# Performance work log

Hardware: AMD Instinct MI355X
Metric: run time of the kernel (lower is better)

The kernel has to match this reference:

```python
import jax, jax.numpy as jnp
import numpy as np

B, N, M, C, H, W = 8, 16, 4, 2, 256, 256
GAMMA = 0.5   # gamma0
BETA = 1.0    # beta
EPS = 1e-8


def setup_inputs() -> dict:
    key = jax.random.key(0)
    k1, k2, k3, k4 = jax.random.split(key, 4)
    gt_arr = jax.random.randint(k1, (B, M, H, W), 0, C)
    sample_arr = jax.random.uniform(k2, (B, N, C, H, W), dtype=jnp.float32)
    prob = jax.random.uniform(k3, (B, N), dtype=jnp.float32)
    prob_gt = jax.random.uniform(k4, (B, M), dtype=jnp.float32)
    prob_gt = prob_gt / prob_gt.sum(-1, keepdims=True)  # gt mixture weights sum to 1
    sample_shape = jnp.array([4, 4], dtype=jnp.int64 if jax.config.read('jax_enable_x64') else jnp.int32)  # (K,S); unused since G0=1
    return {"gt_arr": gt_arr, "sample_arr": sample_arr, "prob": prob,
            "prob_gt": prob_gt, "sample_shape": sample_shape}


def _cost_iou(sample, gt_oh):
    # sample: (B,N,C,HW), gt_oh: (B,M,C,HW) -> cost (B,N,M)
    inter = jnp.einsum('bnch,bmch->bnmc', sample, gt_oh)
    union = sample.sum(-1)[:, :, None, :] + gt_oh.sum(-1)[:, None, :, :] - inter
    # drop background channel 0, mean over remaining channels
    return 1.0 - ((inter + 1.0) / (union + 1.0))[..., 1:].mean(-1)


def _coupling(cost, prob_gt):
    # Greedy sequential OT coupling (gamma != 1 branch), vectorized per gt column
    # via water-filling over cost-sorted samples; sequential over gt columns.
    Bn, Nn, Mn = cost.shape
    mass = 1.0 / Mn

    def per_batch(cb):  # cb: (N,M)
        order_gt = jnp.argsort(cb.min(axis=0))  # gts by their min cost

        def step(carry, i):
            rowsums, P = carry
            col = cb[:, i]                      # (N,)
            ordj = jnp.argsort(col)             # samples by cost for this gt
            caps = GAMMA - rowsums[ordj]        # remaining capacity, >= 0
            excl = jnp.cumsum(caps) - caps      # exclusive prefix of capacities
            a_sorted = jnp.clip(mass - excl, 0.0, caps)
            assign = jnp.zeros((Nn,), cb.dtype).at[ordj].set(a_sorted)
            P = P.at[:, i].set(assign)
            return (rowsums + assign, P), None

        init = (jnp.zeros((Nn,), cb.dtype), jnp.zeros((Nn, Mn), cb.dtype))
        (_, P), _ = jax.lax.scan(step, init, order_gt)
        return P

    P = jax.vmap(per_batch)(cost)
    return P * (prob_gt * Mn)[:, None, :]


def _forward(gt_arr, sample_arr, prob, prob_gt):
    Bn, Nn, Cn, Hn, Wn = sample_arr.shape
    Mn = gt_arr.shape[1]
    sample = sample_arr.reshape(Bn, Nn, Cn, Hn * Wn)
    gt_oh = jnp.transpose(
        jax.nn.one_hot(gt_arr.reshape(Bn, Mn, Hn * Wn), Cn, dtype=sample.dtype),
        (0, 1, 3, 2))                            # (B,M,C,HW)
    cost = _cost_iou(sample, gt_oh)              # (B,N,M)
    P = jax.lax.stop_gradient(_coupling(jax.lax.stop_gradient(cost), prob_gt))
    seg_loss = (P * cost).sum((1, 2)).mean()
    # KL: F.kl_div(log(prob+eps), target_prob) with 'mean' reduction (xlogy at 0)
    target = P.sum(-1)                           # (B,N)
    logp = jnp.log(prob + EPS)
    safe_t = jnp.where(target > 0, target, 1.0)
    kl = jnp.where(target > 0, target * (jnp.log(safe_t) - logp), 0.0).mean()
    loss = seg_loss + BETA * kl
    return loss, seg_loss, kl


def reference(gt_arr, sample_arr, prob, prob_gt, sample_shape):
    return _forward(gt_arr, sample_arr, prob, prob_gt)
```

## Files before the change

kernel.cpp:

```cpp
#include <hip/hip_runtime.h>
#include <math.h>

static constexpr int Bn = 8;
static constexpr int Nn = 16;
static constexpr int Mn = 4;
static constexpr int Cn = 2;
static constexpr int HWn = 256 * 256;
static constexpr int SEGS = 64;
static constexpr int SEGLEN = HWn / SEGS;
#define GAMMA_F 0.5f
#define MASS_F 0.25f
#define EPS_F 1e-8f


__global__ __launch_bounds__(256) void inter2_kernel(
    const float* __restrict__ sample, const int* __restrict__ gt,
    float* __restrict__ inter_part, float* __restrict__ ssum_part,
    float* __restrict__ gsum_part) {
  int seg = blockIdx.x & (SEGS - 1);
  int b = blockIdx.x >> 6;
  int tid = threadIdx.x;
  int w = tid >> 6;
  int lane = tid & 63;
  size_t segoff = (size_t)seg * SEGLEN;

  const int* gtb = gt + ((size_t)b * Mn) * HWn + segoff;
  const float* sb = sample + (size_t)b * Nn * Cn * HWn + HWn + segoff;

  float ss[4] = {0.f, 0.f, 0.f, 0.f};
  float im[4][4] = {};
  float cnt[4] = {0.f, 0.f, 0.f, 0.f};

#pragma unroll
  for (int q = 0; q < 4; ++q) {
    int idx = q * 64 + lane;
    int4 g0 = reinterpret_cast<const int4*>(gtb + 0 * HWn)[idx];
    int4 g1 = reinterpret_cast<const int4*>(gtb + 1 * HWn)[idx];
    int4 g2 = reinterpret_cast<const int4*>(gtb + 2 * HWn)[idx];
    int4 g3 = reinterpret_cast<const int4*>(gtb + 3 * HWn)[idx];
    float mf[4][4];
    {
      int a0[4] = {g0.x, g0.y, g0.z, g0.w};
      int a1[4] = {g1.x, g1.y, g1.z, g1.w};
      int a2[4] = {g2.x, g2.y, g2.z, g2.w};
      int a3[4] = {g3.x, g3.y, g3.z, g3.w};
#pragma unroll
      for (int e = 0; e < 4; ++e) {
        mf[e][0] = (a0[e] == 1) ? 1.f : 0.f;
        mf[e][1] = (a1[e] == 1) ? 1.f : 0.f;
        mf[e][2] = (a2[e] == 1) ? 1.f : 0.f;
        mf[e][3] = (a3[e] == 1) ? 1.f : 0.f;
      }
    }
#pragma unroll
    for (int m = 0; m < 4; ++m)
      cnt[m] += (mf[0][m] + mf[1][m]) + (mf[2][m] + mf[3][m]);
#pragma unroll
    for (int nn = 0; nn < 4; ++nn) {
      const float* spn = sb + (size_t)(w * 4 + nn) * (Cn * HWn);
      float4 x = reinterpret_cast<const float4*>(spn)[idx];
      float xs[4] = {x.x, x.y, x.z, x.w};
#pragma unroll
      for (int e = 0; e < 4; ++e) {
        float v = xs[e];
        ss[nn] += v;
#pragma unroll
        for (int m = 0; m < 4; ++m) im[nn][m] = fmaf(v, mf[e][m], im[nn][m]);
      }
    }
  }

  __shared__ __align__(16) float red[4][20][68];
  __shared__ __align__(16) float redc[4][68];
#pragma unroll
  for (int nn = 0; nn < 4; ++nn) {
    red[w][nn * 5 + 0][lane] = ss[nn];
#pragma unroll
    for (int m = 0; m < 4; ++m) red[w][nn * 5 + 1 + m][lane] = im[nn][m];
  }
  if (w == 0) {
#pragma unroll
    for (int m = 0; m < 4; ++m) redc[m][lane] = cnt[m];
  }
  __syncthreads();

  if (tid < 80) {
    int rw = tid / 20, v = tid % 20;
    const float4* row = reinterpret_cast<const float4*>(&red[rw][v][0]);
    float4 a4 = row[0];
#pragma unroll
    for (int j = 1; j < 16; ++j) {
      float4 t = row[j];
      a4.x += t.x; a4.y += t.y; a4.z += t.z; a4.w += t.w;
    }
    float s = (a4.x + a4.y) + (a4.z + a4.w);
    int n = rw * 4 + v / 5;
    int k = v % 5;
    int bn = b * Nn + n;
    if (k == 0)
      ssum_part[(size_t)bn * SEGS + seg] = s;
    else
      inter_part[((size_t)bn * Mn + (k - 1)) * SEGS + seg] = s;
  } else if (tid < 84) {
    int m = tid - 80;
    const float4* row = reinterpret_cast<const float4*>(&redc[m][0]);
    float4 a4 = row[0];
#pragma unroll
    for (int j = 1; j < 16; ++j) {
      float4 t = row[j];
      a4.x += t.x; a4.y += t.y; a4.z += t.z; a4.w += t.w;
    }
    float s = (a4.x + a4.y) + (a4.z + a4.w);
    gsum_part[((size_t)b * Mn + m) * SEGS + seg] = s;
  }
}

__global__ __launch_bounds__(256) void finish_kernel(
    const float* __restrict__ inter_part, const float* __restrict__ ssum_part,
    const float* __restrict__ gsum_part,
    const float* __restrict__ prob, const float* __restrict__ prob_gt,
    float* __restrict__ out) {
  __shared__ float s_cost[Bn * Nn * Mn];
  __shared__ float s_ssum[Bn * Nn];
  __shared__ float s_gsum[Bn * Mn];
  __shared__ float s_red[8];
  int tid = threadIdx.x;

  if (tid < Bn * Nn) {
    const float4* row = reinterpret_cast<const float4*>(&ssum_part[(size_t)tid * SEGS]);
    float4 a4 = row[0];
#pragma unroll
    for (int j = 1; j < 16; ++j) {
      float4 t = row[j];
      a4.x += t.x; a4.y += t.y; a4.z += t.z; a4.w += t.w;
    }
    s_ssum[tid] = (a4.x + a4.y) + (a4.z + a4.w);
  } else if (tid < 128 + Bn * Mn) {
    int idx = tid - 128;
    const float4* row = reinterpret_cast<const float4*>(&gsum_part[(size_t)idx * SEGS]);
    float4 a4 = row[0];
#pragma unroll
    for (int j = 1; j < 16; ++j) {
      float4 t = row[j];
      a4.x += t.x; a4.y += t.y; a4.z += t.z; a4.w += t.w;
    }
    s_gsum[idx] = (a4.x + a4.y) + (a4.z + a4.w);
  }
  __syncthreads();

  for (int idx = tid; idx < Bn * Nn * Mn; idx += 256) {
    int m = idx & 3;
    int bn = idx >> 2;
    int b = bn >> 4;
    const float4* row = reinterpret_cast<const float4*>(&inter_part[(size_t)idx * SEGS]);
    float4 a4 = row[0];
#pragma unroll
    for (int j = 1; j < 16; ++j) {
      float4 t = row[j];
      a4.x += t.x; a4.y += t.y; a4.z += t.z; a4.w += t.w;
    }
    float inter = (a4.x + a4.y) + (a4.z + a4.w);
    float uni = s_ssum[bn] + s_gsum[(b << 2) + m] - inter;
    s_cost[idx] = 1.0f - (inter + 1.0f) / (uni + 1.0f);
  }
  __syncthreads();

  float seg_part = 0.f, kl_part = 0.f;
  if (tid < Bn * Nn) {
    int b = tid >> 4;
    int n = tid & 15;
    int base = (tid & 63) & ~15;

    float4 cv = *reinterpret_cast<const float4*>(&s_cost[tid * Mn]);
    float cc0 = cv.x, cc1 = cv.y, cc2 = cv.z, cc3 = cv.w;
    float pg0 = prob_gt[b * Mn + 0], pg1 = prob_gt[b * Mn + 1];
    float pg2 = prob_gt[b * Mn + 2], pg3 = prob_gt[b * Mn + 3];

    float m0 = cc0, m1 = cc1, m2 = cc2, m3 = cc3;
#pragma unroll
    for (int off = 1; off < 16; off <<= 1) {
      m0 = fminf(m0, __shfl_xor(m0, off));
      m1 = fminf(m1, __shfl_xor(m1, off));
      m2 = fminf(m2, __shfl_xor(m2, off));
      m3 = fminf(m3, __shfl_xor(m3, off));
    }
    int r0 = (m1 < m0) + (m2 < m0) + (m3 < m0);
    int r1 = (m0 <= m1) + (m2 < m1) + (m3 < m1);
    int r2 = (m0 <= m2) + (m1 <= m2) + (m3 < m2);
    int r3 = (m0 <= m3) + (m1 <= m3) + (m2 <= m3);

    float rowsum = 0.f;
    float target = 0.f;
#pragma unroll
    for (int k = 0; k < Mn; ++k) {
      int i = (r0 == k) ? 0 : (r1 == k) ? 1 : (r2 == k) ? 2 : 3;
      float v = (i == 0) ? cc0 : (i == 1) ? cc1 : (i == 2) ? cc2 : cc3;
      float pg = (i == 0) ? pg0 : (i == 1) ? pg1 : (i == 2) ? pg2 : pg3;
      float cap = GAMMA_F - rowsum;
      float excl = 0.f;
#pragma unroll 4
      for (int j = 0; j < Nn; ++j) {
        float vj = __shfl(v, base + j);
        float capj = __shfl(cap, base + j);
        bool pred = (vj < v) || (vj == v && j < n);
        excl += pred ? capj : 0.f;
      }
      float a = fminf(fmaxf(MASS_F - excl, 0.f), cap);
      rowsum += a;
      float p = a * pg * (float)Mn;
      seg_part += p * v;
      target += p;
    }
    kl_part = (target > 0.f)
                  ? target * (logf(target) - logf(prob[tid] + EPS_F))
                  : 0.f;
  }

#pragma unroll
  for (int off = 32; off > 0; off >>= 1) {
    seg_part += __shfl_down(seg_part, off);
    kl_part += __shfl_down(kl_part, off);
  }
  int lane = tid & 63, wv = tid >> 6;
  if (lane == 0) { s_red[wv * 2] = seg_part; s_red[wv * 2 + 1] = kl_part; }
  __syncthreads();
  if (tid == 0) {
    float seg = 0.f, kl = 0.f;
    for (int w = 0; w < 4; ++w) { seg += s_red[w * 2]; kl += s_red[w * 2 + 1]; }
    seg /= (float)Bn;
    kl /= (float)(Bn * Nn);
    out[0] = seg + 1.0f * kl;
    out[1] = seg;
    out[2] = kl;
  }
}

extern "C" void kernel_launch(void* const* d_in, const int* in_sizes, int n_in,
                              void* d_out, int out_size, void* d_ws, size_t ws_size,
                              hipStream_t stream) {
  const int* gt = (const int*)d_in[0];
  const float* sample = (const float*)d_in[1];
  const float* prob = (const float*)d_in[2];
  const float* prob_gt = (const float*)d_in[3];
  float* out = (float*)d_out;

  char* ws = (char*)d_ws;
  float* inter_part = (float*)(ws + 0);
  float* ssum_part = (float*)(ws + 131072);
  float* gsum_part = (float*)(ws + 163840);

  inter2_kernel<<<Bn * SEGS, 256, 0, stream>>>(sample, gt, inter_part, ssum_part, gsum_part);
  finish_kernel<<<1, 256, 0, stream>>>(inter_part, ssum_part, gsum_part, prob, prob_gt, out);
}
```

Measured before the change: 23.29 us.

## Fuse partial-reduction and finish kernels via cooperative grid sync

Merges the two kernels into one cooperative launch: all blocks write partial sums into a single packed workspace, synchronize with a grid barrier, then block 0 performs the final reduction and greedy coupling. The final row reduction is restructured to use float4 loads with shuffle reductions across 16 lanes. This is meant to remove the second kernel launch and its launch gap, at the cost of a grid-wide barrier and a cooperative launch that requires all 512 blocks to be co-resident.

```diff
diff --git a/kernel.cpp b/kernel.cpp
--- a/kernel.cpp
+++ b/kernel.cpp
@@ -1,5 +1,8 @@
 #include <hip/hip_runtime.h>
+#include <hip/hip_cooperative_groups.h>
 #include <math.h>
+
+namespace cg = cooperative_groups;
 
 static constexpr int Bn = 8;
 static constexpr int Nn = 16;
@@ -12,11 +15,12 @@
 #define MASS_F 0.25f
 #define EPS_F 1e-8f
 
-
-__global__ __launch_bounds__(256) void inter2_kernel(
+static constexpr int ROWS = 672;
+
+__global__ __launch_bounds__(256) void fused_kernel(
     const float* __restrict__ sample, const int* __restrict__ gt,
-    float* __restrict__ inter_part, float* __restrict__ ssum_part,
-    float* __restrict__ gsum_part) {
+    const float* __restrict__ prob, const float* __restrict__ prob_gt,
+    float* __restrict__ part, float* __restrict__ out) {
   int seg = blockIdx.x & (SEGS - 1);
   int b = blockIdx.x >> 6;
   int tid = threadIdx.x;
@@ -97,10 +101,8 @@
     int n = rw * 4 + v / 5;
     int k = v % 5;
     int bn = b * Nn + n;
-    if (k == 0)
-      ssum_part[(size_t)bn * SEGS + seg] = s;
-    else
-      inter_part[((size_t)bn * Mn + (k - 1)) * SEGS + seg] = s;
+    int r = (k == 0) ? (512 + bn) : (bn * Mn + (k - 1));
+    part[(size_t)r * SEGS + seg] = s;
   } else if (tid < 84) {
     int m = tid - 80;
     const float4* row = reinterpret_cast<const float4*>(&redc[m][0]);
@@ -111,70 +113,51 @@
       a4.x += t.x; a4.y += t.y; a4.z += t.z; a4.w += t.w;
     }
     float s = (a4.x + a4.y) + (a4.z + a4.w);
-    gsum_part[((size_t)b * Mn + m) * SEGS + seg] = s;
-  }
-}
-
-__global__ __launch_bounds__(256) void finish_kernel(
-    const float* __restrict__ inter_part, const float* __restrict__ ssum_part,
-    const float* __restrict__ gsum_part,
-    const float* __restrict__ prob, const float* __restrict__ prob_gt,
-    float* __restrict__ out) {
+    part[(size_t)(640 + b * Mn + m) * SEGS + seg] = s;
+  }
+
+  cg::this_grid().sync();
+
+  if (blockIdx.x != 0) return;
+
+  __shared__ float rows[ROWS];
   __shared__ float s_cost[Bn * Nn * Mn];
-  __shared__ float s_ssum[Bn * Nn];
-  __shared__ float s_gsum[Bn * Mn];
   __shared__ float s_red[8];
-  int tid = threadIdx.x;
-
-  if (tid < Bn * Nn) {
-    const float4* row = reinterpret_cast<const float4*>(&ssum_part[(size_t)tid * SEGS]);
-    float4 a4 = row[0];
-#pragma unroll
-    for (int j = 1; j < 16; ++j) {
-      float4 t = row[j];
-      a4.x += t.x; a4.y += t.y; a4.z += t.z; a4.w += t.w;
-    }
-    s_ssum[tid] = (a4.x + a4.y) + (a4.z + a4.w);
-  } else if (tid < 128 + Bn * Mn) {
-    int idx = tid - 128;
-    const float4* row = reinterpret_cast<const float4*>(&gsum_part[(size_t)idx * SEGS]);
-    float4 a4 = row[0];
-#pragma unroll
-    for (int j = 1; j < 16; ++j) {
-      float4 t = row[j];
-      a4.x += t.x; a4.y += t.y; a4.z += t.z; a4.w += t.w;
-    }
-    s_gsum[idx] = (a4.x + a4.y) + (a4.z + a4.w);
+  int wv = tid >> 6;
+
+#pragma unroll 2
+  for (int it = 0; it < ROWS / 16; ++it) {
+    int r0 = it * 16 + wv * 4;
+    float4 x = reinterpret_cast<const float4*>(part)[(size_t)r0 * 16 + lane];
+    float s = (x.x + x.y) + (x.z + x.w);
+    s += __shfl_xor(s, 1);
+    s += __shfl_xor(s, 2);
+    s += __shfl_xor(s, 4);
+    s += __shfl_xor(s, 8);
+    if ((lane & 15) == 0) rows[r0 + (lane >> 4)] = s;
   }
   __syncthreads();
 
   for (int idx = tid; idx < Bn * Nn * Mn; idx += 256) {
     int m = idx & 3;
     int bn = idx >> 2;
-    int b = bn >> 4;
-    const float4* row = reinterpret_cast<const float4*>(&inter_part[(size_t)idx * SEGS]);
-    float4 a4 = row[0];
-#pragma unroll
-    for (int j = 1; j < 16; ++j) {
-      float4 t = row[j];
-      a4.x += t.x; a4.y += t.y; a4.z += t.z; a4.w += t.w;
-    }
-    float inter = (a4.x + a4.y) + (a4.z + a4.w);
-    float uni = s_ssum[bn] + s_gsum[(b << 2) + m] - inter;
+    int bb = bn >> 4;
+    float inter = rows[idx];
+    float uni = rows[512 + bn] + rows[640 + (bb << 2) + m] - inter;
     s_cost[idx] = 1.0f - (inter + 1.0f) / (uni + 1.0f);
   }
   __syncthreads();
 
   float seg_part = 0.f, kl_part = 0.f;
   if (tid < Bn * Nn) {
-    int b = tid >> 4;
+    int bb = tid >> 4;
     int n = tid & 15;
     int base = (tid & 63) & ~15;
 
     float4 cv = *reinterpret_cast<const float4*>(&s_cost[tid * Mn]);
     float cc0 = cv.x, cc1 = cv.y, cc2 = cv.z, cc3 = cv.w;
-    float pg0 = prob_gt[b * Mn + 0], pg1 = prob_gt[b * Mn + 1];
-    float pg2 = prob_gt[b * Mn + 2], pg3 = prob_gt[b * Mn + 3];
+    float pg0 = prob_gt[bb * Mn + 0], pg1 = prob_gt[bb * Mn + 1];
+    float pg2 = prob_gt[bb * Mn + 2], pg3 = prob_gt[bb * Mn + 3];
 
     float m0 = cc0, m1 = cc1, m2 = cc2, m3 = cc3;
 #pragma unroll
@@ -221,16 +204,15 @@
     seg_part += __shfl_down(seg_part, off);
     kl_part += __shfl_down(kl_part, off);
   }
-  int lane = tid & 63, wv = tid >> 6;
   if (lane == 0) { s_red[wv * 2] = seg_part; s_red[wv * 2 + 1] = kl_part; }
   __syncthreads();
   if (tid == 0) {
-    float seg = 0.f, kl = 0.f;
-    for (int w = 0; w < 4; ++w) { seg += s_red[w * 2]; kl += s_red[w * 2 + 1]; }
-    seg /= (float)Bn;
+    float segl = 0.f, kl = 0.f;
+    for (int q = 0; q < 4; ++q) { segl += s_red[q * 2]; kl += s_red[q * 2 + 1]; }
+    segl /= (float)Bn;
     kl /= (float)(Bn * Nn);
-    out[0] = seg + 1.0f * kl;
-    out[1] = seg;
+    out[0] = segl + 1.0f * kl;
+    out[1] = segl;
     out[2] = kl;
   }
 }
@@ -243,12 +225,10 @@
   const float* prob = (const float*)d_in[2];
   const float* prob_gt = (const float*)d_in[3];
   float* out = (float*)d_out;
-
-  char* ws = (char*)d_ws;
-  float* inter_part = (float*)(ws + 0);
-  float* ssum_part = (float*)(ws + 131072);
-  float* gsum_part = (float*)(ws + 163840);
-
-  inter2_kernel<<<Bn * SEGS, 256, 0, stream>>>(sample, gt, inter_part, ssum_part, gsum_part);
-  finish_kernel<<<1, 256, 0, stream>>>(inter_part, ssum_part, gsum_part, prob, prob_gt, out);
+  float* part = (float*)d_ws;
+
+  void* args[] = {(void*)&sample, (void*)&gt, (void*)&prob, (void*)&prob_gt,
+                  (void*)&part, (void*)&out};
+  hipLaunchCooperativeKernel((const void*)fused_kernel, dim3(Bn * SEGS),
+                             dim3(256), args, 0, stream);
 }
```

After: 91.94 us. 295% more time.
